# Kernel optimization log

Measured on AMD Instinct MI355X. Metric: run time of the kernel, lower is better.

## Reference

```python
import jax, jax.numpy as jnp
import numpy as np

N = 8192
INPUT_DIM = 512
R = 2
HID = INPUT_DIM // R  # 256
OUTPUT_DIM = 512


def _linear_params(key, out_dim, in_dim):
    kw, kb = jax.random.split(key)
    bound = 1.0 / np.sqrt(in_dim)
    w = jax.random.uniform(kw, (out_dim, in_dim), jnp.float32, -bound, bound)
    b = jax.random.uniform(kb, (out_dim,), jnp.float32, -bound, bound)
    return w, b


def setup_inputs() -> dict:
    key = jax.random.key(0)
    k0, k1, k2, k3, k4 = jax.random.split(key, 5)
    O0 = jax.random.normal(k0, (N, INPUT_DIM), dtype=jnp.float32)
    W_w, W_b = _linear_params(k1, HID, INPUT_DIM)
    U_w, U_b = _linear_params(k2, HID, INPUT_DIM)
    H_w, H_b = _linear_params(k3, HID, INPUT_DIM)
    fc0_w, fc0_b = _linear_params(k4, OUTPUT_DIM, HID)
    return {"O0": O0, "W_w": W_w, "W_b": W_b, "U_w": U_w, "U_b": U_b,
            "H_w": H_w, "H_b": H_b, "fc0_w": fc0_w, "fc0_b": fc0_b}


def reference(O0, W_w, W_b, U_w, U_b, H_w, H_b, fc0_w, fc0_b):
    q = O0 @ W_w.T + W_b          # [N, HID]
    k = O0 @ U_w.T + U_b          # [N, HID]
    v = O0 @ H_w.T + H_b          # [N, HID]
    # NOTE: no 1/sqrt(d) scaling, faithful to the original module.
    scores = q @ k.T              # [N, N]
    R1 = jax.nn.softmax(scores, axis=1)
    O1 = (R1 @ v) @ fc0_w.T + fc0_b  # [N, OUTPUT_DIM]
    return O1
```

## Files before the change

kernel.cpp:

```cpp
#include <hip/hip_runtime.h>

#define N_TOK 8192
#define IN_DIM 512
#define HID 256
#define OUT_DIM 512

typedef _Float16 v8h __attribute__((ext_vector_type(8)));
typedef float v4f __attribute__((ext_vector_type(4)));

__device__ inline void async_copy16(const void* g, void* l) {
    __builtin_amdgcn_global_load_lds(
        (const __attribute__((address_space(1))) void*)g,
        (__attribute__((address_space(3))) void*)l, 16, 0, 0);
}

__global__ __launch_bounds__(256)
void conv_all(const float* __restrict__ O0, const float* __restrict__ W_w,
              const float* __restrict__ U_w, const float* __restrict__ H_w,
              const float* __restrict__ fc0_w,
              _Float16* __restrict__ O0h, _Float16* __restrict__ Wh,
              _Float16* __restrict__ Uh, _Float16* __restrict__ Hh,
              _Float16* __restrict__ fh) {
    const int b = blockIdx.x;
    const float* src; _Float16* dst; size_t off;
    if (b < 2048) { src = O0; dst = O0h; off = (size_t)b * 2048; }
    else {
        int wsel = (b - 2048) >> 6, wb = (b - 2048) & 63;
        src = (wsel == 0) ? W_w : (wsel == 1) ? U_w : (wsel == 2) ? H_w : fc0_w;
        dst = (wsel == 0) ? Wh  : (wsel == 1) ? Uh  : (wsel == 2) ? Hh  : fh;
        off = (size_t)wb * 2048;
    }
    const size_t i = off + (size_t)threadIdx.x * 8;
    float4 f0 = *(const float4*)&src[i];
    float4 f1 = *(const float4*)&src[i + 4];
    union { _Float16 h[8]; uint4 u; } pk;
    pk.h[0] = (_Float16)f0.x; pk.h[1] = (_Float16)f0.y;
    pk.h[2] = (_Float16)f0.z; pk.h[3] = (_Float16)f0.w;
    pk.h[4] = (_Float16)f1.x; pk.h[5] = (_Float16)f1.y;
    pk.h[6] = (_Float16)f1.z; pk.h[7] = (_Float16)f1.w;
    *(uint4*)&dst[i] = pk.u;
}

__global__ __launch_bounds__(256)
void proj_qkv(const _Float16* __restrict__ O0h,
              const _Float16* __restrict__ Wh, const _Float16* __restrict__ Uh,
              const _Float16* __restrict__ Hh,
              const float* __restrict__ W_b, const float* __restrict__ U_b,
              const float* __restrict__ H_b,
              _Float16* __restrict__ qb, _Float16* __restrict__ kb,
              _Float16* __restrict__ vt) {
    __shared__ _Float16 As[2][128 * 64];
    __shared__ _Float16 Bs[2][64 * 64];

    const int t = threadIdx.x;
    const int wv = t >> 6;
    const int lane = t & 63;
    const int quad = lane >> 4;
    const int lm = lane & 15;
    const int m0 = blockIdx.x * 128;
    const int n0 = blockIdx.y * 64;
    const int z = blockIdx.z;

    const _Float16* Bw  = (z == 0) ? Wh : (z == 1) ? Uh : Hh;
    const float*    bias = (z == 0) ? W_b : (z == 1) ? U_b : H_b;

    auto issue = [&](int k0, int b) {
#pragma unroll
        for (int i = 0; i < 4; i++) {
            int slot = t + 256 * i;
            int r = slot >> 3, cpos = slot & 7;
            int c = (cpos - r) & 7;
            async_copy16(&O0h[(size_t)(m0 + r) * IN_DIM + k0 + c * 8],
                         (_Float16*)As[b] + (size_t)slot * 8);
        }
#pragma unroll
        for (int i = 0; i < 2; i++) {
            int slot = t + 256 * i;
            int r = slot >> 3, cpos = slot & 7;
            int c = (cpos - r) & 7;
            async_copy16(&Bw[(size_t)(n0 + r) * IN_DIM + k0 + c * 8],
                         (_Float16*)Bs[b] + (size_t)slot * 8);
        }
    };

    v4f acc[2][4];
#pragma unroll
    for (int rs = 0; rs < 2; rs++)
#pragma unroll
        for (int ct = 0; ct < 4; ct++) acc[rs][ct] = (v4f){0.f, 0.f, 0.f, 0.f};

    issue(0, 0);
    for (int it = 0; it < IN_DIM / 64; it++) {
        const int buf = it & 1;
        __syncthreads();
        if (it + 1 < IN_DIM / 64) issue((it + 1) * 64, buf ^ 1);

#pragma unroll
        for (int kc = 0; kc < 2; kc++) {
            const int ch = kc * 4 + quad;
            const int rA0 = wv * 32 + lm, rA1 = rA0 + 16;
            v8h a0 = *(const v8h*)(As[buf] + rA0 * 64 + ((ch + rA0) & 7) * 8);
            v8h a1 = *(const v8h*)(As[buf] + rA1 * 64 + ((ch + rA1) & 7) * 8);
            v8h b[4];
#pragma unroll
            for (int ct = 0; ct < 4; ct++) {
                const int rB = ct * 16 + lm;
                b[ct] = *(const v8h*)(Bs[buf] + rB * 64 + ((ch + rB) & 7) * 8);
            }
#pragma unroll
            for (int ct = 0; ct < 4; ct++) {
                acc[0][ct] = __builtin_amdgcn_mfma_f32_16x16x32_f16(a0, b[ct], acc[0][ct], 0, 0, 0);
                acc[1][ct] = __builtin_amdgcn_mfma_f32_16x16x32_f16(a1, b[ct], acc[1][ct], 0, 0, 0);
            }
        }
    }

    if (z < 2) {
        _Float16* outp = (z == 0) ? qb : kb;
#pragma unroll
        for (int rs = 0; rs < 2; rs++)
#pragma unroll
            for (int ct = 0; ct < 4; ct++) {
                const int col = n0 + ct * 16 + lm;
                const float bv = bias[col];
#pragma unroll
                for (int r = 0; r < 4; r++) {
                    const int row = m0 + wv * 32 + rs * 16 + quad * 4 + r;
                    outp[(size_t)row * HID + col] = (_Float16)(acc[rs][ct][r] + bv);
                }
            }
    } else {
#pragma unroll
        for (int rs = 0; rs < 2; rs++)
#pragma unroll
            for (int ct = 0; ct < 4; ct++) {
                const int col = n0 + ct * 16 + lm;
                const float bv = bias[col];
                const int rowbase = m0 + wv * 32 + rs * 16 + quad * 4;
                union { _Float16 h[4]; uint2 u; } pk;
#pragma unroll
                for (int r = 0; r < 4; r++) pk.h[r] = (_Float16)(acc[rs][ct][r] + bv);
                *(uint2*)&vt[(size_t)col * N_TOK + rowbase] = pk.u;
            }
    }
}

__global__ __launch_bounds__(512, 4)
void flash_mfma(const _Float16* __restrict__ qb, const _Float16* __restrict__ kb,
                const _Float16* __restrict__ vt,
                _Float16* __restrict__ partA,
                _Float16* __restrict__ partB,
                float* __restrict__ mbuf, float* __restrict__ lbuf,
                int keys_per_part) {
    __shared__ _Float16 Ks[32 * 256];
    __shared__ _Float16 Vs[2][256 * 32];

    const int t = threadIdx.x;
    const int w = t >> 6;
    const int lane = t & 63;
    const int quad = lane >> 4;
    const int lm = lane & 15;
    const int p = blockIdx.x & 7;
    const int m0 = (blockIdx.x >> 3) * 128 + w * 16;

    _Float16* part = (p < 4) ? partA + (size_t)p * N_TOK * HID
                             : partB + (size_t)(p - 4) * N_TOK * HID;

    v8h aq[8];
#pragma unroll
    for (int c = 0; c < 8; c++)
        aq[c] = *(const v8h*)&qb[(size_t)(m0 + lm) * HID + c * 32 + quad * 8];

    v4f o[16];
    float mr = -1e30f, lr = 0.f;
#pragma unroll
    for (int dt = 0; dt < 16; dt++) o[dt] = (v4f){0.f, 0.f, 0.f, 0.f};

    const int n_start = p * keys_per_part;
    const int iters = keys_per_part / 32;

    auto issue_K = [&](int n0) {
#pragma unroll
        for (int i = 0; i < 2; i++) {
            int slot = t + 512 * i;
            int kr = slot >> 5, cpos = slot & 31;
            int kc = (cpos - kr) & 31;
            int m = kr & 15;
            int src = ((m >> 2) << 3) + ((kr >> 4) << 2) + (m & 3);
            async_copy16(&kb[(size_t)(n0 + src) * HID + kc * 8],
                         (_Float16*)Ks + (size_t)slot * 8);
        }
    };
    auto issue_V = [&](int n0, int b) {
#pragma unroll
        for (int i = 0; i < 2; i++) {
            int slot = t + 512 * i;
            int d = slot >> 2, c = slot & 3;
            async_copy16(&vt[(size_t)d * N_TOK + n0 + c * 8],
                         (_Float16*)Vs[b] + (size_t)slot * 8);
        }
    };

    issue_V(n_start, 0);
    issue_K(n_start);

    for (int it = 0; it < iters; it++) {
        __syncthreads();

        v4f s[2];
        s[0] = (v4f){0.f, 0.f, 0.f, 0.f};
        s[1] = (v4f){0.f, 0.f, 0.f, 0.f};
#pragma unroll
        for (int c = 0; c < 8; c++) {
            const int kc = c * 4 + quad;
            v8h b0 = *(const v8h*)((const _Float16*)Ks + lm * 256 + ((kc + lm) & 31) * 8);
            v8h b1 = *(const v8h*)((const _Float16*)Ks + (16 + lm) * 256 + ((kc + 16 + lm) & 31) * 8);
            s[0] = __builtin_amdgcn_mfma_f32_16x16x32_f16(b0, aq[c], s[0], 0, 0, 0);
            s[1] = __builtin_amdgcn_mfma_f32_16x16x32_f16(b1, aq[c], s[1], 0, 0, 0);
        }

        __syncthreads();
        if (it + 1 < iters) {
            issue_K(n_start + (it + 1) * 32);
            issue_V(n_start + (it + 1) * 32, (it + 1) & 1);
        }

        float tm = s[0][0];
#pragma unroll
        for (int r = 1; r < 4; r++) tm = fmaxf(tm, s[0][r]);
#pragma unroll
        for (int r = 0; r < 4; r++) tm = fmaxf(tm, s[1][r]);
        tm = fmaxf(tm, __shfl_xor(tm, 16));
        tm = fmaxf(tm, __shfl_xor(tm, 32));
        float mn = fmaxf(mr, tm);
        if (__any((int)(mn > mr))) {
            float al = __expf(mr - mn);
            lr *= al;
#pragma unroll
            for (int dt = 0; dt < 16; dt++)
#pragma unroll
                for (int r = 0; r < 4; r++) o[dt][r] *= al;
        }
        mr = mn;
        float ls = 0.f;
        v8h bp;
#pragma unroll
        for (int j = 0; j < 4; j++) {
            float p0 = __expf(s[0][j] - mn);
            float p1 = __expf(s[1][j] - mn);
            bp[j] = (_Float16)p0;
            bp[j + 4] = (_Float16)p1;
            ls += p0 + p1;
        }
        ls += __shfl_xor(ls, 16);
        ls += __shfl_xor(ls, 32);
        lr += ls;

        const _Float16* VsB = (const _Float16*)Vs[it & 1];
#pragma unroll
        for (int dt = 0; dt < 16; dt++) {
            v8h av = *(const v8h*)(VsB + (dt * 16 + lm) * 32 + quad * 8);
            o[dt] = __builtin_amdgcn_mfma_f32_16x16x32_f16(av, bp, o[dt], 0, 0, 0);
        }
    }

    const float inv = 1.0f / lr;
    const int row = m0 + lm;
#pragma unroll
    for (int dt = 0; dt < 16; dt++) {
        union { _Float16 h[4]; uint2 u; } pk;
#pragma unroll
        for (int r = 0; r < 4; r++) pk.h[r] = (_Float16)(o[dt][r] * inv);
        *(uint2*)&part[(size_t)row * HID + dt * 16 + quad * 4] = pk.u;
    }
    if (quad == 0) {
        mbuf[p * N_TOK + row] = mr;
        lbuf[p * N_TOK + row] = lr;
    }
}

__global__ __launch_bounds__(256)
void combine_parts(_Float16* __restrict__ attn,
                   const _Float16* __restrict__ partA, const _Float16* __restrict__ partB,
                   const float* __restrict__ mbuf, const float* __restrict__ lbuf,
                   int P) {
    const int gid = blockIdx.x * 256 + threadIdx.x;
    const int row = gid >> 5;
    const int c8 = (gid & 31) * 8;

    float M = -1e30f;
    for (int p = 0; p < P; p++) M = fmaxf(M, mbuf[p * N_TOK + row]);
    float den = 0.f;
    float acc[8];
#pragma unroll
    for (int j = 0; j < 8; j++) acc[j] = 0.f;
    for (int p = 0; p < P; p++) {
        float wgt = lbuf[p * N_TOK + row] * __expf(mbuf[p * N_TOK + row] - M);
        den += wgt;
        const _Float16* base = (p < 4) ? partA + (size_t)p * N_TOK * HID
                                       : partB + (size_t)(p - 4) * N_TOK * HID;
        v8h y = *(const v8h*)&base[(size_t)row * HID + c8];
#pragma unroll
        for (int j = 0; j < 8; j++) acc[j] += wgt * (float)y[j];
    }
    const float inv = 1.0f / den;
    union { _Float16 h[8]; uint4 u; } pk;
#pragma unroll
    for (int j = 0; j < 8; j++) pk.h[j] = (_Float16)(acc[j] * inv);
    *(uint4*)&attn[(size_t)row * HID + c8] = pk.u;
}

__global__ __launch_bounds__(256)
void mfma_fc0(const _Float16* __restrict__ Ah, const _Float16* __restrict__ Bh,
              const float* __restrict__ bias, float* __restrict__ Cout) {
    __shared__ _Float16 As[2][128 * 64];
    __shared__ _Float16 Bs[2][64 * 64];

    const int t = threadIdx.x;
    const int wv = t >> 6;
    const int lane = t & 63;
    const int quad = lane >> 4;
    const int lm = lane & 15;
    const int m0 = blockIdx.x * 128;
    const int n0 = blockIdx.y * 64;

    auto issue = [&](int k0, int b) {
#pragma unroll
        for (int i = 0; i < 4; i++) {
            int slot = t + 256 * i;
            int r = slot >> 3, cpos = slot & 7;
            int c = (cpos - r) & 7;
            async_copy16(&Ah[(size_t)(m0 + r) * HID + k0 + c * 8],
                         (_Float16*)As[b] + (size_t)slot * 8);
        }
#pragma unroll
        for (int i = 0; i < 2; i++) {
            int slot = t + 256 * i;
            int r = slot >> 3, cpos = slot & 7;
            int c = (cpos - r) & 7;
            async_copy16(&Bh[(size_t)(n0 + r) * HID + k0 + c * 8],
                         (_Float16*)Bs[b] + (size_t)slot * 8);
        }
    };

    v4f acc[2][4];
#pragma unroll
    for (int rs = 0; rs < 2; rs++)
#pragma unroll
        for (int ct = 0; ct < 4; ct++) acc[rs][ct] = (v4f){0.f, 0.f, 0.f, 0.f};

    issue(0, 0);
    for (int it = 0; it < HID / 64; it++) {
        const int buf = it & 1;
        __syncthreads();
        if (it + 1 < HID / 64) issue((it + 1) * 64, buf ^ 1);

#pragma unroll
        for (int kc = 0; kc < 2; kc++) {
            const int ch = kc * 4 + quad;
            const int rA0 = wv * 32 + lm, rA1 = rA0 + 16;
            v8h a0 = *(const v8h*)(As[buf] + rA0 * 64 + ((ch + rA0) & 7) * 8);
            v8h a1 = *(const v8h*)(As[buf] + rA1 * 64 + ((ch + rA1) & 7) * 8);
            v8h b[4];
#pragma unroll
            for (int ct = 0; ct < 4; ct++) {
                const int rB = ct * 16 + lm;
                b[ct] = *(const v8h*)(Bs[buf] + rB * 64 + ((ch + rB) & 7) * 8);
            }
#pragma unroll
            for (int ct = 0; ct < 4; ct++) {
                acc[0][ct] = __builtin_amdgcn_mfma_f32_16x16x32_f16(a0, b[ct], acc[0][ct], 0, 0, 0);
                acc[1][ct] = __builtin_amdgcn_mfma_f32_16x16x32_f16(a1, b[ct], acc[1][ct], 0, 0, 0);
            }
        }
    }

#pragma unroll
    for (int rs = 0; rs < 2; rs++)
#pragma unroll
        for (int ct = 0; ct < 4; ct++) {
            const int col = n0 + ct * 16 + lm;
            const float bv = bias[col];
#pragma unroll
            for (int r = 0; r < 4; r++) {
                const int row = m0 + wv * 32 + rs * 16 + quad * 4 + r;
                Cout[(size_t)row * OUT_DIM + col] = acc[rs][ct][r] + bv;
            }
        }
}

extern "C" void kernel_launch(void* const* d_in, const int* in_sizes, int n_in,
                              void* d_out, int out_size, void* d_ws, size_t ws_size,
                              hipStream_t stream) {
    const float* O0    = (const float*)d_in[0];
    const float* W_w   = (const float*)d_in[1];
    const float* W_b   = (const float*)d_in[2];
    const float* U_w   = (const float*)d_in[3];
    const float* U_b   = (const float*)d_in[4];
    const float* H_w   = (const float*)d_in[5];
    const float* H_b   = (const float*)d_in[6];
    const float* fc0_w = (const float*)d_in[7];
    const float* fc0_b = (const float*)d_in[8];

    char* ws = (char*)d_ws;
    _Float16* qb    = (_Float16*)ws;
    _Float16* kb    = (_Float16*)(ws + ((size_t)4 << 20));
    _Float16* vt    = (_Float16*)(ws + ((size_t)8 << 20));
    float*    mbuf  = (float*)(ws + ((size_t)12 << 20));
    float*    lbuf  = mbuf + 8 * N_TOK;
    _Float16* Wh    = (_Float16*)(ws + ((size_t)12 << 20) + ((size_t)512 << 10));
    _Float16* Uh    = Wh + (size_t)HID * IN_DIM;
    _Float16* Hh    = Uh + (size_t)HID * IN_DIM;
    _Float16* fh    = Hh + (size_t)HID * IN_DIM;
    _Float16* partB = (_Float16*)(ws + ((size_t)16 << 20));
    _Float16* attn  = qb;
    _Float16* O0h   = (_Float16*)d_out;
    _Float16* partA = (_Float16*)d_out;

    const int P = 8;
    const int kpp = N_TOK / P;

    conv_all<<<dim3(2048 + 256), dim3(256), 0, stream>>>(
        O0, W_w, U_w, H_w, fc0_w, O0h, Wh, Uh, Hh, fh);

    proj_qkv<<<dim3(N_TOK / 128, HID / 64, 3), dim3(256), 0, stream>>>(
        O0h, Wh, Uh, Hh, W_b, U_b, H_b, qb, kb, vt);

    flash_mfma<<<dim3((N_TOK / 128) * P), dim3(512), 0, stream>>>(
        qb, kb, vt, partA, partB, mbuf, lbuf, kpp);

    combine_parts<<<dim3(N_TOK * HID / 8 / 256), dim3(256), 0, stream>>>(
        attn, partA, partB, mbuf, lbuf, P);

    mfma_fc0<<<dim3(N_TOK / 128, OUT_DIM / 64), dim3(256), 0, stream>>>(
        attn, fh, fc0_b, (float*)d_out);
}
```

Measured before the change: 234.7 us.

## Give each flash wave 32 query rows, double-buffer K, compute row sums via MFMA

The flash attention kernel drops from 8 to 4 waves per block, and each wave now handles two 16-row query slices. Each K and V fragment read from LDS is reused across both slices, halving LDS reads per MFMA. K gets a second LDS buffer, so the next tile's loads are issued right after the barrier instead of after the QK step, removing one barrier per iteration. The softmax denominator is now accumulated by an MFMA against a ones vector instead of shuffle reductions. The cost is roughly double the accumulator registers per wave and fewer waves for latency hiding.

```diff
diff --git a/kernel.cpp b/kernel.cpp
--- a/kernel.cpp
+++ b/kernel.cpp
@@ -145,14 +145,14 @@
     }
 }
 
-__global__ __launch_bounds__(512, 4)
+__global__ __launch_bounds__(256, 2)
 void flash_mfma(const _Float16* __restrict__ qb, const _Float16* __restrict__ kb,
                 const _Float16* __restrict__ vt,
                 _Float16* __restrict__ partA,
                 _Float16* __restrict__ partB,
                 float* __restrict__ mbuf, float* __restrict__ lbuf,
                 int keys_per_part) {
-    __shared__ _Float16 Ks[32 * 256];
+    __shared__ _Float16 Ks[2][32 * 256];
     __shared__ _Float16 Vs[2][256 * 32];
 
     const int t = threadIdx.x;
@@ -161,121 +161,144 @@
     const int quad = lane >> 4;
     const int lm = lane & 15;
     const int p = blockIdx.x & 7;
-    const int m0 = (blockIdx.x >> 3) * 128 + w * 16;
+    const int m0 = (blockIdx.x >> 3) * 128 + w * 32;
 
     _Float16* part = (p < 4) ? partA + (size_t)p * N_TOK * HID
                              : partB + (size_t)(p - 4) * N_TOK * HID;
 
-    v8h aq[8];
-#pragma unroll
-    for (int c = 0; c < 8; c++)
-        aq[c] = *(const v8h*)&qb[(size_t)(m0 + lm) * HID + c * 32 + quad * 8];
-
-    v4f o[16];
-    float mr = -1e30f, lr = 0.f;
-#pragma unroll
-    for (int dt = 0; dt < 16; dt++) o[dt] = (v4f){0.f, 0.f, 0.f, 0.f};
+    v8h aq[2][8];
+#pragma unroll
+    for (int rs = 0; rs < 2; rs++)
+#pragma unroll
+        for (int c = 0; c < 8; c++)
+            aq[rs][c] = *(const v8h*)&qb[(size_t)(m0 + rs * 16 + lm) * HID + c * 32 + quad * 8];
+
+    v8h vone;
+#pragma unroll
+    for (int j = 0; j < 8; j++) vone[j] = (_Float16)1.0f;
+
+    v4f o[2][16];
+    v4f lacc[2];
+    float mr[2];
+#pragma unroll
+    for (int rs = 0; rs < 2; rs++) {
+#pragma unroll
+        for (int dt = 0; dt < 16; dt++) o[rs][dt] = (v4f){0.f, 0.f, 0.f, 0.f};
+        lacc[rs] = (v4f){0.f, 0.f, 0.f, 0.f};
+        mr[rs] = -1e30f;
+    }
 
     const int n_start = p * keys_per_part;
     const int iters = keys_per_part / 32;
 
-    auto issue_K = [&](int n0) {
-#pragma unroll
-        for (int i = 0; i < 2; i++) {
-            int slot = t + 512 * i;
+    auto issue_K = [&](int n0, int b) {
+#pragma unroll
+        for (int i = 0; i < 4; i++) {
+            int slot = t + 256 * i;
             int kr = slot >> 5, cpos = slot & 31;
             int kc = (cpos - kr) & 31;
             int m = kr & 15;
             int src = ((m >> 2) << 3) + ((kr >> 4) << 2) + (m & 3);
             async_copy16(&kb[(size_t)(n0 + src) * HID + kc * 8],
-                         (_Float16*)Ks + (size_t)slot * 8);
+                         (_Float16*)Ks[b] + (size_t)slot * 8);
         }
     };
     auto issue_V = [&](int n0, int b) {
 #pragma unroll
-        for (int i = 0; i < 2; i++) {
-            int slot = t + 512 * i;
+        for (int i = 0; i < 4; i++) {
+            int slot = t + 256 * i;
             int d = slot >> 2, c = slot & 3;
             async_copy16(&vt[(size_t)d * N_TOK + n0 + c * 8],
                          (_Float16*)Vs[b] + (size_t)slot * 8);
         }
     };
 
+    issue_K(n_start, 0);
     issue_V(n_start, 0);
-    issue_K(n_start);
 
     for (int it = 0; it < iters; it++) {
+        const int buf = it & 1;
         __syncthreads();
-
-        v4f s[2];
-        s[0] = (v4f){0.f, 0.f, 0.f, 0.f};
-        s[1] = (v4f){0.f, 0.f, 0.f, 0.f};
+        if (it + 1 < iters) {
+            issue_K(n_start + (it + 1) * 32, buf ^ 1);
+            issue_V(n_start + (it + 1) * 32, buf ^ 1);
+        }
+
+        const _Float16* KsB = (const _Float16*)Ks[buf];
+        const _Float16* VsB = (const _Float16*)Vs[buf];
+
+        v4f s[2][2];
+#pragma unroll
+        for (int rs = 0; rs < 2; rs++)
+#pragma unroll
+            for (int nt = 0; nt < 2; nt++) s[rs][nt] = (v4f){0.f, 0.f, 0.f, 0.f};
 #pragma unroll
         for (int c = 0; c < 8; c++) {
             const int kc = c * 4 + quad;
-            v8h b0 = *(const v8h*)((const _Float16*)Ks + lm * 256 + ((kc + lm) & 31) * 8);
-            v8h b1 = *(const v8h*)((const _Float16*)Ks + (16 + lm) * 256 + ((kc + 16 + lm) & 31) * 8);
-            s[0] = __builtin_amdgcn_mfma_f32_16x16x32_f16(b0, aq[c], s[0], 0, 0, 0);
-            s[1] = __builtin_amdgcn_mfma_f32_16x16x32_f16(b1, aq[c], s[1], 0, 0, 0);
-        }
-
-        __syncthreads();
-        if (it + 1 < iters) {
-            issue_K(n_start + (it + 1) * 32);
-            issue_V(n_start + (it + 1) * 32, (it + 1) & 1);
-        }
-
-        float tm = s[0][0];
-#pragma unroll
-        for (int r = 1; r < 4; r++) tm = fmaxf(tm, s[0][r]);
-#pragma unroll
-        for (int r = 0; r < 4; r++) tm = fmaxf(tm, s[1][r]);
-        tm = fmaxf(tm, __shfl_xor(tm, 16));
-        tm = fmaxf(tm, __shfl_xor(tm, 32));
-        float mn = fmaxf(mr, tm);
-        if (__any((int)(mn > mr))) {
-            float al = __expf(mr - mn);
-            lr *= al;
-#pragma unroll
-            for (int dt = 0; dt < 16; dt++)
-#pragma unroll
-                for (int r = 0; r < 4; r++) o[dt][r] *= al;
-        }
-        mr = mn;
-        float ls = 0.f;
-        v8h bp;
-#pragma unroll
-        for (int j = 0; j < 4; j++) {
-            float p0 = __expf(s[0][j] - mn);
-            float p1 = __expf(s[1][j] - mn);
-            bp[j] = (_Float16)p0;
-            bp[j + 4] = (_Float16)p1;
-            ls += p0 + p1;
-        }
-        ls += __shfl_xor(ls, 16);
-        ls += __shfl_xor(ls, 32);
-        lr += ls;
-
-        const _Float16* VsB = (const _Float16*)Vs[it & 1];
+            v8h b0 = *(const v8h*)(KsB + lm * 256 + ((kc + lm) & 31) * 8);
+            v8h b1 = *(const v8h*)(KsB + (16 + lm) * 256 + ((kc + 16 + lm) & 31) * 8);
+            s[0][0] = __builtin_amdgcn_mfma_f32_16x16x32_f16(b0, aq[0][c], s[0][0], 0, 0, 0);
+            s[0][1] = __builtin_amdgcn_mfma_f32_16x16x32_f16(b1, aq[0][c], s[0][1], 0, 0, 0);
+            s[1][0] = __builtin_amdgcn_mfma_f32_16x16x32_f16(b0, aq[1][c], s[1][0], 0, 0, 0);
+            s[1][1] = __builtin_amdgcn_mfma_f32_16x16x32_f16(b1, aq[1][c], s[1][1], 0, 0, 0);
+        }
+
+        v8h bp[2];
+#pragma unroll
+        for (int rs = 0; rs < 2; rs++) {
+            float tm = s[rs][0][0];
+#pragma unroll
+            for (int r = 1; r < 4; r++) tm = fmaxf(tm, s[rs][0][r]);
+#pragma unroll
+            for (int r = 0; r < 4; r++) tm = fmaxf(tm, s[rs][1][r]);
+            tm = fmaxf(tm, __shfl_xor(tm, 16));
+            tm = fmaxf(tm, __shfl_xor(tm, 32));
+            float mn = fmaxf(mr[rs], tm);
+            if (__any((int)(mn > mr[rs]))) {
+                float al = __expf(mr[rs] - mn);
+#pragma unroll
+                for (int r = 0; r < 4; r++) lacc[rs][r] *= al;
+#pragma unroll
+                for (int dt = 0; dt < 16; dt++)
+#pragma unroll
+                    for (int r = 0; r < 4; r++) o[rs][dt][r] *= al;
+            }
+            mr[rs] = mn;
+            v8h bpv;
+#pragma unroll
+            for (int j = 0; j < 4; j++) {
+                bpv[j]     = (_Float16)__expf(s[rs][0][j] - mn);
+                bpv[j + 4] = (_Float16)__expf(s[rs][1][j] - mn);
+            }
+            bp[rs] = bpv;
+        }
+
+        lacc[0] = __builtin_amdgcn_mfma_f32_16x16x32_f16(vone, bp[0], lacc[0], 0, 0, 0);
+        lacc[1] = __builtin_amdgcn_mfma_f32_16x16x32_f16(vone, bp[1], lacc[1], 0, 0, 0);
 #pragma unroll
         for (int dt = 0; dt < 16; dt++) {
             v8h av = *(const v8h*)(VsB + (dt * 16 + lm) * 32 + quad * 8);
-            o[dt] = __builtin_amdgcn_mfma_f32_16x16x32_f16(av, bp, o[dt], 0, 0, 0);
-        }
-    }
-
-    const float inv = 1.0f / lr;
-    const int row = m0 + lm;
-#pragma unroll
-    for (int dt = 0; dt < 16; dt++) {
-        union { _Float16 h[4]; uint2 u; } pk;
-#pragma unroll
-        for (int r = 0; r < 4; r++) pk.h[r] = (_Float16)(o[dt][r] * inv);
-        *(uint2*)&part[(size_t)row * HID + dt * 16 + quad * 4] = pk.u;
-    }
-    if (quad == 0) {
-        mbuf[p * N_TOK + row] = mr;
-        lbuf[p * N_TOK + row] = lr;
+            o[0][dt] = __builtin_amdgcn_mfma_f32_16x16x32_f16(av, bp[0], o[0][dt], 0, 0, 0);
+            o[1][dt] = __builtin_amdgcn_mfma_f32_16x16x32_f16(av, bp[1], o[1][dt], 0, 0, 0);
+        }
+    }
+
+#pragma unroll
+    for (int rs = 0; rs < 2; rs++) {
+        const float lr = lacc[rs][0];
+        const float inv = 1.0f / lr;
+        const int row = m0 + rs * 16 + lm;
+#pragma unroll
+        for (int dt = 0; dt < 16; dt++) {
+            union { _Float16 h[4]; uint2 u; } pk;
+#pragma unroll
+            for (int r = 0; r < 4; r++) pk.h[r] = (_Float16)(o[rs][dt][r] * inv);
+            *(uint2*)&part[(size_t)row * HID + dt * 16 + quad * 4] = pk.u;
+        }
+        if (quad == 0) {
+            mbuf[p * N_TOK + row] = mr[rs];
+            lbuf[p * N_TOK + row] = lr;
+        }
     }
 }
 
@@ -426,7 +449,7 @@
     proj_qkv<<<dim3(N_TOK / 128, HID / 64, 3), dim3(256), 0, stream>>>(
         O0h, Wh, Uh, Hh, W_b, U_b, H_b, qb, kb, vt);
 
-    flash_mfma<<<dim3((N_TOK / 128) * P), dim3(512), 0, stream>>>(
+    flash_mfma<<<dim3((N_TOK / 128) * P), dim3(256), 0, stream>>>(
         qb, kb, vt, partA, partB, mbuf, lbuf, kpp);
 
     combine_parts<<<dim3(N_TOK * HID / 8 / 256), dim3(256), 0, stream>>>(
```

Measured after the change: 216.3 us. -7.8%, faster.
